# Optimization experiments

Measured on AMD Instinct MI355X. Metric: run time of the kernel, lower is better.

## Reference

```python
import jax, jax.numpy as jnp
import numpy as np

BN_EPS = 1e-5

def _bn(h, gamma, beta):
    # training-mode BatchNorm1d: batch stats over node axis
    mu = h.mean(0)
    var = h.var(0)
    return (h - mu) * jax.lax.rsqrt(var + BN_EPS) * gamma + beta

def setup_inputs() -> dict:
    key = jax.random.key(0)
    ks = jax.random.split(key, 12)
    N, E, NF, EF = 100000, 3200000, 16, 8
    x = jax.random.normal(ks[0], (N, NF), jnp.float32)
    edge_index = jax.random.randint(ks[1], (2, E), 0, N, jnp.int64)
    edge_attr = jax.random.normal(ks[2], (E, EF), jnp.float32)
    s = 0.1
    params = dict(
        We=jax.random.normal(ks[3], (EF, NF), jnp.float32) * s,
        be=jnp.zeros((NF,), jnp.float32),
        W1=jax.random.normal(ks[4], (NF, 32), jnp.float32) * s,
        b1=jnp.zeros((32,), jnp.float32),
        g1=jnp.ones((32,), jnp.float32),
        bt1=jnp.zeros((32,), jnp.float32),
        W2=jax.random.normal(ks[5], (32, 32), jnp.float32) * s,
        b2=jnp.zeros((32,), jnp.float32),
        eps=jnp.float32(0.0),
        g2=jnp.ones((32,), jnp.float32),
        bt2=jnp.zeros((32,), jnp.float32),
        W3=jax.random.normal(ks[6], (32, 64), jnp.float32) * s,
        b3=jnp.zeros((64,), jnp.float32),
    )
    return dict(x=x, edge_index=edge_index, edge_attr=edge_attr, **params)

def reference(x, edge_index, edge_attr, We, be, W1, b1, g1, bt1, W2, b2, eps, g2, bt2, W3, b3):
    N = x.shape[0]
    src, dst = edge_index[0], edge_index[1]
    # GINEConv: project edge_attr to node dim, message = ReLU(x_src + e)
    e = edge_attr @ We + be                      # [E, NF]
    msg = jax.nn.relu(x[src] + e)                # [E, NF]  (gather)
    agg = jax.ops.segment_sum(msg, dst, num_segments=N)  # [N, NF] (scatter-sum)
    h = (1.0 + eps) * x + agg
    # nn1: Linear -> BN -> GELU -> Linear
    h = h @ W1 + b1
    h = jax.nn.gelu(_bn(h, g1, bt1), approximate=False)
    h = h @ W2 + b2                              # [N, 32]
    # post-conv: BN -> GELU -> Linear(32,64)
    h = jax.nn.gelu(_bn(h, g2, bt2), approximate=False)
    return h @ W3 + b3                           # [N, 64]
```

## Files before the change

### kernel.cpp

```cpp
#include <hip/hip_runtime.h>
#include <math.h>

#define NF 16
#define EF 8
#define H1D 32
#define H2D 32
#define OD 64

__device__ __forceinline__ float gelu_exact(float t) {
    return 0.5f * t * (1.0f + erff(t * 0.70710678118654752440f));
}

__global__ __launch_bounds__(256) void k_hist(
    const int* __restrict__ ei, int* __restrict__ count, int* __restrict__ pos,
    int N, int E)
{
    int e = blockIdx.x * 256 + threadIdx.x;
    if (e >= E) return;
    int dst = ei[(size_t)E + e];
    if ((unsigned)dst >= (unsigned)N) { pos[e] = -1; return; }
    pos[e] = atomicAdd(&count[dst], 1);
}

#define SCAN_T 1024
__global__ __launch_bounds__(SCAN_T) void k_scan(
    const int* __restrict__ count, int* __restrict__ rowptr, int N)
{
    __shared__ int part[SCAN_T];
    int t = threadIdx.x;
    int C = (N + SCAN_T - 1) / SCAN_T;
    int lo = min(t * C, N), hi = min(lo + C, N);
    int s = 0;
    for (int i = lo; i < hi; ++i) s += count[i];
    part[t] = s;
    __syncthreads();
    for (int off = 1; off < SCAN_T; off <<= 1) {
        int v = (t >= off) ? part[t - off] : 0;
        __syncthreads();
        part[t] += v;
        __syncthreads();
    }
    int run = (t == 0) ? 0 : part[t - 1];
    for (int i = lo; i < hi; ++i) { rowptr[i] = run; run += count[i]; }
    if (t == SCAN_T - 1) rowptr[N] = part[SCAN_T - 1];
}

__global__ __launch_bounds__(256) void k_scatter(
    const int* __restrict__ ei, const int* __restrict__ rowptr,
    const int* __restrict__ pos, int* __restrict__ eids, int N, int E)
{
    int e = blockIdx.x * 256 + threadIdx.x;
    if (e >= E) return;
    int dst = ei[(size_t)E + e];
    if ((unsigned)dst >= (unsigned)N) return;
    int p = pos[e];
    if (p < 0) return;
    eids[rowptr[dst] + p] = e;
}

__global__ __launch_bounds__(256) void k_gather(
    const float* __restrict__ x, const int* __restrict__ ei,
    const float* __restrict__ ea, const float* __restrict__ We,
    const float* __restrict__ be, const int* __restrict__ rowptr,
    const int* __restrict__ eids, float* __restrict__ agg, int N, int E)
{
    int wid = (blockIdx.x * 256 + threadIdx.x) >> 6;
    int lane = threadIdx.x & 63;
    if (wid >= N) return;
    int f = lane & 15, g = lane >> 4;

    float w[EF];
#pragma unroll
    for (int k = 0; k < EF; ++k) w[k] = We[k * NF + f];
    float bef = be[f];

    int r0 = rowptr[wid], r1 = rowptr[wid + 1];
    float acc = 0.0f;
    for (int t = r0 + g; t < r1; t += 4) {
        int e = eids[t];
        if ((unsigned)e >= (unsigned)E) continue;
        int src = ei[e];
        if ((unsigned)src >= (unsigned)N) continue;
        const float4* ea4 = reinterpret_cast<const float4*>(ea + (size_t)e * EF);
        float4 a0 = ea4[0], a1 = ea4[1];
        float ev = bef;
        ev += a0.x * w[0] + a0.y * w[1] + a0.z * w[2] + a0.w * w[3]
            + a1.x * w[4] + a1.y * w[5] + a1.z * w[6] + a1.w * w[7];
        acc += fmaxf(x[(size_t)src * NF + f] + ev, 0.0f);
    }
    acc += __shfl_xor(acc, 16);
    acc += __shfl_xor(acc, 32);
    if (g == 0) agg[(size_t)wid * NF + f] = acc;
}

__global__ __launch_bounds__(256) void k_edge(
    const float* __restrict__ x, const int* __restrict__ ei,
    const float* __restrict__ ea, const float* __restrict__ We,
    const float* __restrict__ be, float* __restrict__ agg, int N, int E)
{
    __shared__ float sWe[EF * NF];
    __shared__ float sbe[NF];
    int t = threadIdx.x;
    if (t < EF * NF) sWe[t] = We[t];
    if (t < NF) sbe[t] = be[t];
    __syncthreads();
    int e = blockIdx.x * 256 + t;
    if (e >= E) return;
    int src = ei[e];
    int dst = ei[(size_t)E + e];
    if ((unsigned)src >= (unsigned)N || (unsigned)dst >= (unsigned)N) return;
    const float4* ea4 = reinterpret_cast<const float4*>(ea + (size_t)e * EF);
    float4 a0 = ea4[0], a1 = ea4[1];
    float ak[EF] = {a0.x, a0.y, a0.z, a0.w, a1.x, a1.y, a1.z, a1.w};
    const float4* sbe4 = reinterpret_cast<const float4*>(sbe);
    float4 ev[4] = {sbe4[0], sbe4[1], sbe4[2], sbe4[3]};
    const float4* sWe4 = reinterpret_cast<const float4*>(sWe);
#pragma unroll
    for (int k = 0; k < EF; ++k) {
        float a = ak[k];
#pragma unroll
        for (int j = 0; j < 4; ++j) {
            float4 wv = sWe4[k * 4 + j];
            ev[j].x += a * wv.x; ev[j].y += a * wv.y;
            ev[j].z += a * wv.z; ev[j].w += a * wv.w;
        }
    }
    const float4* xs = reinterpret_cast<const float4*>(x + (size_t)src * NF);
    float* ad = agg + (size_t)dst * NF;
#pragma unroll
    for (int j = 0; j < 4; ++j) {
        float4 xv = xs[j];
        atomicAdd(ad + j * 4 + 0, fmaxf(xv.x + ev[j].x, 0.0f));
        atomicAdd(ad + j * 4 + 1, fmaxf(xv.y + ev[j].y, 0.0f));
        atomicAdd(ad + j * 4 + 2, fmaxf(xv.z + ev[j].z, 0.0f));
        atomicAdd(ad + j * 4 + 3, fmaxf(xv.w + ev[j].w, 0.0f));
    }
}

__global__ __launch_bounds__(256) void k_nodeA(
    const float* __restrict__ x, const float* __restrict__ agg,
    const float* __restrict__ W1, const float* __restrict__ b1,
    const float* __restrict__ epsp, float* __restrict__ h1,
    float* __restrict__ partial, int N)
{
    __shared__ float sW1[NF * H1D];
    __shared__ float sb1[H1D];
    __shared__ float sred[4][H1D], qred[4][H1D];
    int t = threadIdx.x;
    for (int i = t; i < NF * H1D; i += 256) sW1[i] = W1[i];
    if (t < H1D) sb1[t] = b1[t];
    __syncthreads();

    int i = blockIdx.x * 256 + t;
    bool active = i < N;
    float onep = 1.0f + epsp[0];
    int w = t >> 6;

    float acc[H1D];
    if (active) {
        float h0[NF];
        const float4* xs = reinterpret_cast<const float4*>(x + (size_t)i * NF);
        const float4* as = reinterpret_cast<const float4*>(agg + (size_t)i * NF);
#pragma unroll
        for (int j = 0; j < 4; ++j) {
            float4 xv = xs[j], av = as[j];
            h0[4 * j + 0] = onep * xv.x + av.x;
            h0[4 * j + 1] = onep * xv.y + av.y;
            h0[4 * j + 2] = onep * xv.z + av.z;
            h0[4 * j + 3] = onep * xv.w + av.w;
        }
#pragma unroll
        for (int j = 0; j < H1D; ++j) acc[j] = sb1[j];
#pragma unroll
        for (int k = 0; k < NF; ++k) {
            float a = h0[k];
#pragma unroll
            for (int j = 0; j < H1D; ++j) acc[j] += a * sW1[k * H1D + j];
        }
        float4* o = reinterpret_cast<float4*>(h1 + (size_t)i * H1D);
#pragma unroll
        for (int j = 0; j < 8; ++j)
            o[j] = make_float4(acc[4 * j + 0], acc[4 * j + 1], acc[4 * j + 2], acc[4 * j + 3]);
    } else {
#pragma unroll
        for (int j = 0; j < H1D; ++j) acc[j] = 0.0f;
    }

#pragma unroll
    for (int j = 0; j < H1D; ++j) {
        float s = acc[j];
        float q = s * s;
#pragma unroll
        for (int off = 32; off; off >>= 1) {
            s += __shfl_xor(s, off);
            q += __shfl_xor(q, off);
        }
        if ((t & 63) == 0) { sred[w][j] = s; qred[w][j] = q; }
    }
    __syncthreads();
    float* pb = partial + (size_t)blockIdx.x * 64;
    if (t < H1D)
        pb[t] = sred[0][t] + sred[1][t] + sred[2][t] + sred[3][t];
    else if (t < 64)
        pb[t] = qred[0][t - 32] + qred[1][t - 32] + qred[2][t - 32] + qred[3][t - 32];
}

__global__ __launch_bounds__(256) void k_red(
    const float* __restrict__ partial, int rows,
    const float* __restrict__ g, const float* __restrict__ bt,
    float* __restrict__ stats, int N)
{
    __shared__ float acc[4][64];
    int t = threadIdx.x;
    int c = t & 63, r0 = t >> 6;
    float s = 0.0f;
    for (int r = r0; r < rows; r += 4) s += partial[(size_t)r * 64 + c];
    acc[r0][c] = s;
    __syncthreads();
    if (t < 64) acc[0][t] = acc[0][t] + acc[1][t] + acc[2][t] + acc[3][t];
    __syncthreads();
    if (t < 32) {
        float sum = acc[0][t], sq = acc[0][32 + t];
        float mu = sum / (float)N;
        float var = sq / (float)N - mu * mu;
        float inv = rsqrtf(var + 1e-5f);
        float scale = g[t] * inv;
        float shift = bt[t] - mu * scale;
        stats[t] = scale;
        stats[32 + t] = shift;
    }
}

__global__ __launch_bounds__(256) void k_nodeB(
    const float* __restrict__ h1, const float* __restrict__ st1,
    const float* __restrict__ W2, const float* __restrict__ b2,
    float* __restrict__ h2, float* __restrict__ partial, int N)
{
    __shared__ float sW2[H1D * H2D];
    __shared__ float sb2[H2D], ssc[H1D], ssh[H1D];
    __shared__ float sred[4][H2D], qred[4][H2D];
    int t = threadIdx.x;
    for (int i = t; i < H1D * H2D; i += 256) sW2[i] = W2[i];
    if (t < H2D) sb2[t] = b2[t];
    if (t < H1D) { ssc[t] = st1[t]; ssh[t] = st1[H1D + t]; }
    __syncthreads();

    int i = blockIdx.x * 256 + t;
    bool active = i < N;
    int w = t >> 6;

    float acc[H2D];
    if (active) {
        float tg[H1D];
        const float4* hs = reinterpret_cast<const float4*>(h1 + (size_t)i * H1D);
#pragma unroll
        for (int j = 0; j < 8; ++j) {
            float4 v = hs[j];
            tg[4 * j + 0] = gelu_exact(v.x * ssc[4 * j + 0] + ssh[4 * j + 0]);
            tg[4 * j + 1] = gelu_exact(v.y * ssc[4 * j + 1] + ssh[4 * j + 1]);
            tg[4 * j + 2] = gelu_exact(v.z * ssc[4 * j + 2] + ssh[4 * j + 2]);
            tg[4 * j + 3] = gelu_exact(v.w * ssc[4 * j + 3] + ssh[4 * j + 3]);
        }
#pragma unroll
        for (int j = 0; j < H2D; ++j) acc[j] = sb2[j];
#pragma unroll
        for (int k = 0; k < H1D; ++k) {
            float a = tg[k];
#pragma unroll
            for (int j = 0; j < H2D; ++j) acc[j] += a * sW2[k * H2D + j];
        }
        float4* o = reinterpret_cast<float4*>(h2 + (size_t)i * H2D);
#pragma unroll
        for (int j = 0; j < 8; ++j)
            o[j] = make_float4(acc[4 * j + 0], acc[4 * j + 1], acc[4 * j + 2], acc[4 * j + 3]);
    } else {
#pragma unroll
        for (int j = 0; j < H2D; ++j) acc[j] = 0.0f;
    }

#pragma unroll
    for (int j = 0; j < H2D; ++j) {
        float s = acc[j];
        float q = s * s;
#pragma unroll
        for (int off = 32; off; off >>= 1) {
            s += __shfl_xor(s, off);
            q += __shfl_xor(q, off);
        }
        if ((t & 63) == 0) { sred[w][j] = s; qred[w][j] = q; }
    }
    __syncthreads();
    float* pb = partial + (size_t)blockIdx.x * 64;
    if (t < H2D)
        pb[t] = sred[0][t] + sred[1][t] + sred[2][t] + sred[3][t];
    else if (t < 64)
        pb[t] = qred[0][t - 32] + qred[1][t - 32] + qred[2][t - 32] + qred[3][t - 32];
}

__global__ __launch_bounds__(256) void k_nodeC(
    const float* __restrict__ h2, const float* __restrict__ st2,
    const float* __restrict__ W3, const float* __restrict__ b3,
    float* __restrict__ out, int N)
{
    __shared__ float sW3[H2D * OD];
    __shared__ float sb3[OD], ssc[H2D], ssh[H2D];
    int t = threadIdx.x;
    for (int i = t; i < H2D * OD; i += 256) sW3[i] = W3[i];
    if (t < OD) sb3[t] = b3[t];
    if (t < H2D) { ssc[t] = st2[t]; ssh[t] = st2[H2D + t]; }
    __syncthreads();

    int i = blockIdx.x * 256 + t;
    if (i >= N) return;

    float tg[H2D];
    const float4* hs = reinterpret_cast<const float4*>(h2 + (size_t)i * H2D);
#pragma unroll
    for (int j = 0; j < 8; ++j) {
        float4 v = hs[j];
        tg[4 * j + 0] = gelu_exact(v.x * ssc[4 * j + 0] + ssh[4 * j + 0]);
        tg[4 * j + 1] = gelu_exact(v.y * ssc[4 * j + 1] + ssh[4 * j + 1]);
        tg[4 * j + 2] = gelu_exact(v.z * ssc[4 * j + 2] + ssh[4 * j + 2]);
        tg[4 * j + 3] = gelu_exact(v.w * ssc[4 * j + 3] + ssh[4 * j + 3]);
    }
    float acc[OD];
#pragma unroll
    for (int j = 0; j < OD; ++j) acc[j] = sb3[j];
#pragma unroll
    for (int k = 0; k < H2D; ++k) {
        float a = tg[k];
#pragma unroll
        for (int j = 0; j < OD; ++j) acc[j] += a * sW3[k * OD + j];
    }
    float4* o = reinterpret_cast<float4*>(out + (size_t)i * OD);
#pragma unroll
    for (int j = 0; j < 16; ++j)
        o[j] = make_float4(acc[4 * j + 0], acc[4 * j + 1], acc[4 * j + 2], acc[4 * j + 3]);
}

extern "C" void kernel_launch(void* const* d_in, const int* in_sizes, int n_in,
                              void* d_out, int out_size, void* d_ws, size_t ws_size,
                              hipStream_t stream) {
    const float* x   = (const float*)d_in[0];
    const int*   ei  = (const int*)d_in[1];
    const float* ea  = (const float*)d_in[2];
    const float* We  = (const float*)d_in[3];
    const float* be  = (const float*)d_in[4];
    const float* W1  = (const float*)d_in[5];
    const float* b1  = (const float*)d_in[6];
    const float* g1  = (const float*)d_in[7];
    const float* bt1 = (const float*)d_in[8];
    const float* W2  = (const float*)d_in[9];
    const float* b2  = (const float*)d_in[10];
    const float* epsp= (const float*)d_in[11];
    const float* g2  = (const float*)d_in[12];
    const float* bt2 = (const float*)d_in[13];
    const float* W3  = (const float*)d_in[14];
    const float* b3  = (const float*)d_in[15];

    int N = in_sizes[0] / NF;
    int E = in_sizes[2] / EF;
    float* out = (float*)d_out;

    int ebl = (E + 255) / 256;
    int nbl = (N + 255) / 256;
    int gbl = (N + 3) / 4;

    char* ws = (char*)d_ws;
    size_t aggB  = (size_t)N * NF * sizeof(float);
    size_t hB    = (size_t)N * H1D * sizeof(float);
    size_t cntB  = (size_t)N * sizeof(int);
    size_t rpB   = (size_t)(N + 1) * sizeof(int);
    size_t eB    = (size_t)E * sizeof(int);
    size_t statB = 512;
    size_t partB = (size_t)nbl * 64 * sizeof(float);

    size_t coreB = aggB + 2 * hB + cntB + rpB + statB + 2 * partB;
    size_t fullB = coreB + 2 * eB;

    if (ws_size >= coreB && (ws_size >= fullB || (size_t)out_size * sizeof(float) >= 2 * eB)) {
        char* p = ws;
        float* agg    = (float*)p; p += aggB;
        float* h1     = (float*)p; p += hB;
        float* h2     = (float*)p; p += hB;
        int*   count  = (int*)p;   p += cntB;
        int*   rowptr = (int*)p;   p += rpB;
        float* stats1 = (float*)p; p += statB;
        float* stats2 = stats1 + 64;
        float* part1  = (float*)p; p += partB;
        float* part2  = (float*)p; p += partB;
        int *pos, *eids;
        if (ws_size >= fullB) {
            pos  = (int*)p;
            eids = (int*)(p + eB);
        } else {
            pos  = (int*)d_out;
            eids = (int*)((char*)d_out + eB);
        }

        hipMemsetAsync(count, 0, cntB, stream);

        k_hist<<<ebl, 256, 0, stream>>>(ei, count, pos, N, E);
        k_scan<<<1, SCAN_T, 0, stream>>>(count, rowptr, N);
        k_scatter<<<ebl, 256, 0, stream>>>(ei, rowptr, pos, eids, N, E);
        k_gather<<<gbl, 256, 0, stream>>>(x, ei, ea, We, be, rowptr, eids, agg, N, E);
        k_nodeA<<<nbl, 256, 0, stream>>>(x, agg, W1, b1, epsp, h1, part1, N);
        k_red<<<1, 256, 0, stream>>>(part1, nbl, g1, bt1, stats1, N);
        k_nodeB<<<nbl, 256, 0, stream>>>(h1, stats1, W2, b2, h2, part2, N);
        k_red<<<1, 256, 0, stream>>>(part2, nbl, g2, bt2, stats2, N);
        k_nodeC<<<nbl, 256, 0, stream>>>(h2, stats2, W3, b3, out, N);
    } else {
        char* p = ws;
        float* agg = (float*)p; p += aggB;
        float *h1, *h2;
        if (ws_size >= aggB + 2 * hB + statB + 2 * partB) {
            h1 = (float*)p; p += hB;
            h2 = (float*)p; p += hB;
        } else {
            h1 = out;
            h2 = (float*)p; p += hB;
        }
        float* stats1 = (float*)p; p += statB;
        float* stats2 = stats1 + 64;
        float* part1  = (float*)p; p += partB;
        float* part2  = (float*)p; p += partB;

        hipMemsetAsync(agg, 0, aggB, stream);

        k_edge<<<ebl, 256, 0, stream>>>(x, ei, ea, We, be, agg, N, E);
        k_nodeA<<<nbl, 256, 0, stream>>>(x, agg, W1, b1, epsp, h1, part1, N);
        k_red<<<1, 256, 0, stream>>>(part1, nbl, g1, bt1, stats1, N);
        k_nodeB<<<nbl, 256, 0, stream>>>(h1, stats1, W2, b2, h2, part2, N);
        k_red<<<1, 256, 0, stream>>>(part2, nbl, g2, bt2, stats2, N);
        k_nodeC<<<nbl, 256, 0, stream>>>(h2, stats2, W3, b3, out, N);
    }
}
```

Measured before the change: 816.4 us.

## Compute edge messages in edge order and write them to CSR slots, then gather sequentially

Result: slower. 904.5 us (+10.8%).

```diff
diff --git a/kernel.cpp b/kernel.cpp
--- a/kernel.cpp
+++ b/kernel.cpp
@@ -45,17 +45,78 @@
     if (t == SCAN_T - 1) rowptr[N] = part[SCAN_T - 1];
 }
 
-__global__ __launch_bounds__(256) void k_scatter(
-    const int* __restrict__ ei, const int* __restrict__ rowptr,
-    const int* __restrict__ pos, int* __restrict__ eids, int N, int E)
-{
-    int e = blockIdx.x * 256 + threadIdx.x;
+__global__ __launch_bounds__(256) void k_scatmsg(
+    const float* __restrict__ x, const int* __restrict__ ei,
+    const float* __restrict__ ea, const float* __restrict__ We,
+    const float* __restrict__ be, const int* __restrict__ rowptr,
+    const int* __restrict__ pos, float* __restrict__ msg, int N, int E)
+{
+    __shared__ float sWe[EF * NF];
+    __shared__ float sbe[NF];
+    int t = threadIdx.x;
+    if (t < EF * NF) sWe[t] = We[t];
+    if (t < NF) sbe[t] = be[t];
+    __syncthreads();
+
+    int e = blockIdx.x * 256 + t;
     if (e >= E) return;
     int dst = ei[(size_t)E + e];
     if ((unsigned)dst >= (unsigned)N) return;
     int p = pos[e];
     if (p < 0) return;
-    eids[rowptr[dst] + p] = e;
+    size_t slot = (size_t)rowptr[dst] + p;
+    float4* mo = reinterpret_cast<float4*>(msg + slot * NF);
+
+    int src = ei[e];
+    if ((unsigned)src >= (unsigned)N) {
+        float4 z = make_float4(0.f, 0.f, 0.f, 0.f);
+        mo[0] = z; mo[1] = z; mo[2] = z; mo[3] = z;
+        return;
+    }
+
+    const float4* ea4 = reinterpret_cast<const float4*>(ea + (size_t)e * EF);
+    float4 a0 = ea4[0], a1 = ea4[1];
+    float ak[EF] = {a0.x, a0.y, a0.z, a0.w, a1.x, a1.y, a1.z, a1.w};
+    const float4* sbe4 = reinterpret_cast<const float4*>(sbe);
+    float4 ev[4] = {sbe4[0], sbe4[1], sbe4[2], sbe4[3]};
+    const float4* sWe4 = reinterpret_cast<const float4*>(sWe);
+#pragma unroll
+    for (int k = 0; k < EF; ++k) {
+        float a = ak[k];
+#pragma unroll
+        for (int j = 0; j < 4; ++j) {
+            float4 wv = sWe4[k * 4 + j];
+            ev[j].x += a * wv.x; ev[j].y += a * wv.y;
+            ev[j].z += a * wv.z; ev[j].w += a * wv.w;
+        }
+    }
+    const float4* xs = reinterpret_cast<const float4*>(x + (size_t)src * NF);
+#pragma unroll
+    for (int j = 0; j < 4; ++j) {
+        float4 xv = xs[j];
+        mo[j] = make_float4(fmaxf(xv.x + ev[j].x, 0.0f),
+                            fmaxf(xv.y + ev[j].y, 0.0f),
+                            fmaxf(xv.z + ev[j].z, 0.0f),
+                            fmaxf(xv.w + ev[j].w, 0.0f));
+    }
+}
+
+__global__ __launch_bounds__(256) void k_gatherseq(
+    const int* __restrict__ rowptr, const float* __restrict__ msg,
+    float* __restrict__ agg, int N)
+{
+    int wid = (blockIdx.x * 256 + threadIdx.x) >> 6;
+    int lane = threadIdx.x & 63;
+    if (wid >= N) return;
+    int f = lane & 15, g = lane >> 4;
+
+    int r0 = rowptr[wid], r1 = rowptr[wid + 1];
+    float acc = 0.0f;
+    for (int t = r0 + g; t < r1; t += 4)
+        acc += msg[(size_t)t * NF + f];
+    acc += __shfl_xor(acc, 16);
+    acc += __shfl_xor(acc, 32);
+    if (g == 0) agg[(size_t)wid * NF + f] = acc;
 }
 
 __global__ __launch_bounds__(256) void k_gather(
@@ -91,6 +152,19 @@
     acc += __shfl_xor(acc, 16);
     acc += __shfl_xor(acc, 32);
     if (g == 0) agg[(size_t)wid * NF + f] = acc;
+}
+
+__global__ __launch_bounds__(256) void k_scatter(
+    const int* __restrict__ ei, const int* __restrict__ rowptr,
+    const int* __restrict__ pos, int* __restrict__ eids, int N, int E)
+{
+    int e = blockIdx.x * 256 + threadIdx.x;
+    if (e >= E) return;
+    int dst = ei[(size_t)E + e];
+    if ((unsigned)dst >= (unsigned)N) return;
+    int p = pos[e];
+    if (p < 0) return;
+    eids[rowptr[dst] + p] = e;
 }
 
 __global__ __launch_bounds__(256) void k_edge(
@@ -372,13 +446,41 @@
     size_t cntB  = (size_t)N * sizeof(int);
     size_t rpB   = (size_t)(N + 1) * sizeof(int);
     size_t eB    = (size_t)E * sizeof(int);
+    size_t msgB  = (size_t)E * NF * sizeof(float);
     size_t statB = 512;
     size_t partB = (size_t)nbl * 64 * sizeof(float);
 
     size_t coreB = aggB + 2 * hB + cntB + rpB + statB + 2 * partB;
-    size_t fullB = coreB + 2 * eB;
-
-    if (ws_size >= coreB && (ws_size >= fullB || (size_t)out_size * sizeof(float) >= 2 * eB)) {
+    size_t tierA = coreB + eB + msgB;
+    size_t tierB = coreB + 2 * eB;
+
+    if (ws_size >= tierA) {
+        char* p = ws;
+        float* agg    = (float*)p; p += aggB;
+        float* h1     = (float*)p; p += hB;
+        float* h2     = (float*)p; p += hB;
+        float* msg    = (float*)p; p += msgB;
+        int*   pos    = (int*)p;   p += eB;
+        int*   count  = (int*)p;   p += cntB;
+        int*   rowptr = (int*)p;   p += rpB;
+        float* stats1 = (float*)p; p += statB;
+        float* stats2 = stats1 + 64;
+        float* part1  = (float*)p; p += partB;
+        float* part2  = (float*)p; p += partB;
+
+        hipMemsetAsync(count, 0, cntB, stream);
+
+        k_hist<<<ebl, 256, 0, stream>>>(ei, count, pos, N, E);
+        k_scan<<<1, SCAN_T, 0, stream>>>(count, rowptr, N);
+        k_scatmsg<<<ebl, 256, 0, stream>>>(x, ei, ea, We, be, rowptr, pos, msg, N, E);
+        k_gatherseq<<<gbl, 256, 0, stream>>>(rowptr, msg, agg, N);
+        k_nodeA<<<nbl, 256, 0, stream>>>(x, agg, W1, b1, epsp, h1, part1, N);
+        k_red<<<1, 256, 0, stream>>>(part1, nbl, g1, bt1, stats1, N);
+        k_nodeB<<<nbl, 256, 0, stream>>>(h1, stats1, W2, b2, h2, part2, N);
+        k_red<<<1, 256, 0, stream>>>(part2, nbl, g2, bt2, stats2, N);
+        k_nodeC<<<nbl, 256, 0, stream>>>(h2, stats2, W3, b3, out, N);
+    } else if (ws_size >= coreB &&
+               (ws_size >= tierB || (size_t)out_size * sizeof(float) >= 2 * eB)) {
         char* p = ws;
         float* agg    = (float*)p; p += aggB;
         float* h1     = (float*)p; p += hB;
@@ -390,7 +492,7 @@
         float* part1  = (float*)p; p += partB;
         float* part2  = (float*)p; p += partB;
         int *pos, *eids;
-        if (ws_size >= fullB) {
+        if (ws_size >= tierB) {
             pos  = (int*)p;
             eids = (int*)(p + eB);
         } else {
```

## Replace per-node CSR gather with binned edge partition and LDS atomic aggregation

Applied to the files above, without the earlier changes.

Result: no change. 805.3 us (-1.4%).

```diff
diff --git a/kernel.cpp b/kernel.cpp
--- a/kernel.cpp
+++ b/kernel.cpp
@@ -6,23 +6,52 @@
 #define H1D 32
 #define H2D 32
 #define OD 64
+#define PB 256
+#define BNODE 256
+#define SCAN_T 1024
+
+typedef float f32x4 __attribute__((ext_vector_type(4)));
 
 __device__ __forceinline__ float gelu_exact(float t) {
     return 0.5f * t * (1.0f + erff(t * 0.70710678118654752440f));
 }
 
-__global__ __launch_bounds__(256) void k_hist(
-    const int* __restrict__ ei, int* __restrict__ count, int* __restrict__ pos,
-    int N, int E)
-{
-    int e = blockIdx.x * 256 + threadIdx.x;
-    if (e >= E) return;
-    int dst = ei[(size_t)E + e];
-    if ((unsigned)dst >= (unsigned)N) { pos[e] = -1; return; }
-    pos[e] = atomicAdd(&count[dst], 1);
-}
-
-#define SCAN_T 1024
+__global__ __launch_bounds__(256) void k_count(
+    const int* __restrict__ ei, int* __restrict__ cnt, int N, int E, int NBIN, int per)
+{
+    extern __shared__ int lh[];
+    int b = blockIdx.x, t = threadIdx.x;
+    for (int i = t; i < NBIN; i += 256) lh[i] = 0;
+    __syncthreads();
+    int lo = b * per, hi = min(lo + per, E);
+    for (int e = lo + t; e < hi; e += 256) {
+        int dst = ei[(size_t)E + e];
+        int src = ei[e];
+        if ((unsigned)dst < (unsigned)N && (unsigned)src < (unsigned)N)
+            atomicAdd(&lh[dst >> 8], 1);
+    }
+    __syncthreads();
+    for (int i = t; i < NBIN; i += 256) cnt[(size_t)b * NBIN + i] = lh[i];
+}
+
+__global__ __launch_bounds__(256) void k_mscan(
+    const int* __restrict__ cnt, int* __restrict__ off, int* __restrict__ coltot, int NBIN)
+{
+    __shared__ int sh[256];
+    int bin = blockIdx.x, t = threadIdx.x;
+    int v = cnt[(size_t)t * NBIN + bin];
+    sh[t] = v;
+    __syncthreads();
+    for (int o = 1; o < 256; o <<= 1) {
+        int u = (t >= o) ? sh[t - o] : 0;
+        __syncthreads();
+        sh[t] += u;
+        __syncthreads();
+    }
+    off[(size_t)t * NBIN + bin] = sh[t] - v;
+    if (t == 255) coltot[bin] = sh[255];
+}
+
 __global__ __launch_bounds__(SCAN_T) void k_scan(
     const int* __restrict__ count, int* __restrict__ rowptr, int N)
 {
@@ -45,49 +74,173 @@
     if (t == SCAN_T - 1) rowptr[N] = part[SCAN_T - 1];
 }
 
-__global__ __launch_bounds__(256) void k_scatter(
-    const int* __restrict__ ei, const int* __restrict__ rowptr,
-    const int* __restrict__ pos, int* __restrict__ eids, int N, int E)
+__global__ __launch_bounds__(256) void k_place(
+    const int* __restrict__ ei, const float* __restrict__ ea,
+    const int* __restrict__ off, const int* __restrict__ binbase,
+    unsigned* __restrict__ srcpk, float* __restrict__ ea8,
+    int N, int E, int NBIN, int per)
+{
+    extern __shared__ int lc[];
+    int b = blockIdx.x, t = threadIdx.x;
+    for (int i = t; i < NBIN; i += 256) lc[i] = 0;
+    __syncthreads();
+    int lo = b * per, hi = min(lo + per, E);
+    for (int e = lo + t; e < hi; e += 256) {
+        int dst = ei[(size_t)E + e];
+        int src = ei[e];
+        if ((unsigned)dst >= (unsigned)N || (unsigned)src >= (unsigned)N) continue;
+        int bin = dst >> 8;
+        int pos = atomicAdd(&lc[bin], 1);
+        int slot = binbase[bin] + off[(size_t)b * NBIN + bin] + pos;
+        srcpk[slot] = ((unsigned)(dst & 255) << 24) | (unsigned)src;
+        const f32x4* s4 = reinterpret_cast<const f32x4*>(ea + (size_t)e * EF);
+        f32x4 a0 = s4[0], a1 = s4[1];
+        f32x4* d4 = reinterpret_cast<f32x4*>(ea8 + (size_t)slot * EF);
+        d4[0] = a0; d4[1] = a1;
+    }
+}
+
+__global__ __launch_bounds__(256) void k_binagg(
+    const float* __restrict__ x, const unsigned* __restrict__ srcpk,
+    const float* __restrict__ ea8, const float* __restrict__ We,
+    const float* __restrict__ be, const int* __restrict__ binbase,
+    float* __restrict__ agg2, int N)
+{
+    __shared__ float sWe[EF * NF];
+    __shared__ float sbe[NF];
+    __shared__ float as[NF * BNODE];
+    int t = threadIdx.x;
+    int bin = blockIdx.x >> 1, s = blockIdx.x & 1;
+    if (t < EF * NF) sWe[t] = We[t];
+    if (t < NF) sbe[t] = be[t];
+    for (int i = t; i < NF * BNODE; i += 256) as[i] = 0.0f;
+    __syncthreads();
+
+    int lo = binbase[bin], hi = binbase[bin + 1];
+    int half = (hi - lo) >> 1;
+    int l0 = s ? (lo + half) : lo;
+    int h0 = s ? hi : (lo + half);
+
+    const f32x4* sw = reinterpret_cast<const f32x4*>(sWe);
+    const f32x4* sb4 = reinterpret_cast<const f32x4*>(sbe);
+    for (int idx = l0 + t; idx < h0; idx += 256) {
+        unsigned u = srcpk[idx];
+        int src = (int)(u & 0xFFFFFFu);
+        int doff = (int)(u >> 24);
+        const f32x4* e4 = reinterpret_cast<const f32x4*>(ea8 + (size_t)idx * EF);
+        f32x4 a0 = e4[0], a1 = e4[1];
+        float ak[EF] = {a0[0], a0[1], a0[2], a0[3], a1[0], a1[1], a1[2], a1[3]};
+        f32x4 ev[4] = {sb4[0], sb4[1], sb4[2], sb4[3]};
+#pragma unroll
+        for (int k = 0; k < EF; ++k) {
+            float a = ak[k];
+#pragma unroll
+            for (int j = 0; j < 4; ++j) ev[j] += a * sw[k * 4 + j];
+        }
+        const f32x4* xs = reinterpret_cast<const f32x4*>(x + (size_t)src * NF);
+#pragma unroll
+        for (int j = 0; j < 4; ++j) {
+            f32x4 xv = xs[j];
+#pragma unroll
+            for (int c = 0; c < 4; ++c) {
+                float m = fmaxf(xv[c] + ev[j][c], 0.0f);
+                atomicAdd(&as[(j * 4 + c) * BNODE + doff], m);
+            }
+        }
+    }
+    __syncthreads();
+
+    float* ag = agg2 + (size_t)s * (size_t)N * NF;
+    int node = bin * BNODE + t;
+    if (t < BNODE && node < N) {
+        f32x4* o = reinterpret_cast<f32x4*>(ag + (size_t)node * NF);
+#pragma unroll
+        for (int j = 0; j < 4; ++j) {
+            f32x4 v;
+#pragma unroll
+            for (int c = 0; c < 4; ++c) v[c] = as[(j * 4 + c) * BNODE + t];
+            o[j] = v;
+        }
+    }
+}
+
+__global__ __launch_bounds__(256) void k_histp(
+    const int* __restrict__ ei, int* __restrict__ count, unsigned* __restrict__ packed,
+    int N, int E)
 {
     int e = blockIdx.x * 256 + threadIdx.x;
     if (e >= E) return;
     int dst = ei[(size_t)E + e];
-    if ((unsigned)dst >= (unsigned)N) return;
-    int p = pos[e];
-    if (p < 0) return;
-    eids[rowptr[dst] + p] = e;
-}
-
-__global__ __launch_bounds__(256) void k_gather(
+    if ((unsigned)dst >= (unsigned)N || dst >= (1 << 20)) { packed[e] = 0xFFFFFFFFu; return; }
+    int p = atomicAdd(&count[dst], 1);
+    if (p > 4095) p = 4095;
+    packed[e] = ((unsigned)p << 20) | (unsigned)dst;
+}
+
+__global__ __launch_bounds__(256) void k_scatmsg(
     const float* __restrict__ x, const int* __restrict__ ei,
     const float* __restrict__ ea, const float* __restrict__ We,
     const float* __restrict__ be, const int* __restrict__ rowptr,
-    const int* __restrict__ eids, float* __restrict__ agg, int N, int E)
+    const unsigned* __restrict__ packed, float* __restrict__ msg, int N, int E)
+{
+    __shared__ float sWe[EF * NF];
+    __shared__ float sbe[NF];
+    int t = threadIdx.x;
+    if (t < EF * NF) sWe[t] = We[t];
+    if (t < NF) sbe[t] = be[t];
+    __syncthreads();
+
+    int e = blockIdx.x * 256 + t;
+    if (e >= E) return;
+    unsigned u = packed[e];
+    if (u == 0xFFFFFFFFu) return;
+    int dst = (int)(u & 0xFFFFFu);
+    int p   = (int)(u >> 20);
+    size_t slot = (size_t)rowptr[dst] + p;
+    f32x4* mo = reinterpret_cast<f32x4*>(msg + slot * NF);
+
+    int src = ei[e];
+    if ((unsigned)src >= (unsigned)N) {
+        f32x4 z = (f32x4)0.0f;
+        mo[0] = z; mo[1] = z; mo[2] = z; mo[3] = z;
+        return;
+    }
+    const f32x4* ea4 = reinterpret_cast<const f32x4*>(ea + (size_t)e * EF);
+    f32x4 a01 = __builtin_nontemporal_load(ea4 + 0);
+    f32x4 a23 = __builtin_nontemporal_load(ea4 + 1);
+    float ak[EF] = {a01[0], a01[1], a01[2], a01[3], a23[0], a23[1], a23[2], a23[3]};
+    const f32x4* sbe4 = reinterpret_cast<const f32x4*>(sbe);
+    f32x4 ev[4] = {sbe4[0], sbe4[1], sbe4[2], sbe4[3]};
+    const f32x4* sWe4 = reinterpret_cast<const f32x4*>(sWe);
+#pragma unroll
+    for (int k = 0; k < EF; ++k) {
+        float a = ak[k];
+#pragma unroll
+        for (int j = 0; j < 4; ++j) ev[j] += a * sWe4[k * 4 + j];
+    }
+    const f32x4* xs = reinterpret_cast<const f32x4*>(x + (size_t)src * NF);
+#pragma unroll
+    for (int j = 0; j < 4; ++j) {
+        f32x4 xv = xs[j];
+        f32x4 m;
+#pragma unroll
+        for (int c = 0; c < 4; ++c) m[c] = fmaxf(xv[c] + ev[j][c], 0.0f);
+        mo[j] = m;
+    }
+}
+
+__global__ __launch_bounds__(256) void k_gatherseq(
+    const int* __restrict__ rowptr, const float* __restrict__ msg,
+    float* __restrict__ agg, int N)
 {
     int wid = (blockIdx.x * 256 + threadIdx.x) >> 6;
     int lane = threadIdx.x & 63;
     if (wid >= N) return;
     int f = lane & 15, g = lane >> 4;
-
-    float w[EF];
-#pragma unroll
-    for (int k = 0; k < EF; ++k) w[k] = We[k * NF + f];
-    float bef = be[f];
-
     int r0 = rowptr[wid], r1 = rowptr[wid + 1];
     float acc = 0.0f;
-    for (int t = r0 + g; t < r1; t += 4) {
-        int e = eids[t];
-        if ((unsigned)e >= (unsigned)E) continue;
-        int src = ei[e];
-        if ((unsigned)src >= (unsigned)N) continue;
-        const float4* ea4 = reinterpret_cast<const float4*>(ea + (size_t)e * EF);
-        float4 a0 = ea4[0], a1 = ea4[1];
-        float ev = bef;
-        ev += a0.x * w[0] + a0.y * w[1] + a0.z * w[2] + a0.w * w[3]
-            + a1.x * w[4] + a1.y * w[5] + a1.z * w[6] + a1.w * w[7];
-        acc += fmaxf(x[(size_t)src * NF + f] + ev, 0.0f);
-    }
+    for (int t = r0 + g; t < r1; t += 4)
+        acc += __builtin_nontemporal_load(msg + (size_t)t * NF + f);
     acc += __shfl_xor(acc, 16);
     acc += __shfl_xor(acc, 32);
     if (g == 0) agg[(size_t)wid * NF + f] = acc;
@@ -138,7 +291,8 @@
 }
 
 __global__ __launch_bounds__(256) void k_nodeA(
-    const float* __restrict__ x, const float* __restrict__ agg,
+    const float* __restrict__ x, const float* __restrict__ aggL,
+    const float* __restrict__ aggH,
     const float* __restrict__ W1, const float* __restrict__ b1,
     const float* __restrict__ epsp, float* __restrict__ h1,
     float* __restrict__ partial, int N)
@@ -160,14 +314,16 @@
     if (active) {
         float h0[NF];
         const float4* xs = reinterpret_cast<const float4*>(x + (size_t)i * NF);
-        const float4* as = reinterpret_cast<const float4*>(agg + (size_t)i * NF);
+        const float4* aL = reinterpret_cast<const float4*>(aggL + (size_t)i * NF);
+        const float4* aH = aggH ? reinterpret_cast<const float4*>(aggH + (size_t)i * NF) : nullptr;
 #pragma unroll
         for (int j = 0; j < 4; ++j) {
-            float4 xv = xs[j], av = as[j];
-            h0[4 * j + 0] = onep * xv.x + av.x;
-            h0[4 * j + 1] = onep * xv.y + av.y;
-            h0[4 * j + 2] = onep * xv.z + av.z;
-            h0[4 * j + 3] = onep * xv.w + av.w;
+            float4 xv = xs[j], av = aL[j];
+            float4 bv = aH ? aH[j] : make_float4(0.f, 0.f, 0.f, 0.f);
+            h0[4 * j + 0] = onep * xv.x + av.x + bv.x;
+            h0[4 * j + 1] = onep * xv.y + av.y + bv.y;
+            h0[4 * j + 2] = onep * xv.z + av.z + bv.z;
+            h0[4 * j + 3] = onep * xv.w + av.w + bv.w;
         }
 #pragma unroll
         for (int j = 0; j < H1D; ++j) acc[j] = sb1[j];
@@ -365,73 +521,98 @@
     int ebl = (E + 255) / 256;
     int nbl = (N + 255) / 256;
     int gbl = (N + 3) / 4;
+    int NBIN = (N + BNODE - 1) / BNODE;
+    int per  = (E + PB - 1) / PB;
+
+    auto al = [](size_t v) { return (v + 63) & ~(size_t)63; };
 
     char* ws = (char*)d_ws;
-    size_t aggB  = (size_t)N * NF * sizeof(float);
-    size_t hB    = (size_t)N * H1D * sizeof(float);
-    size_t cntB  = (size_t)N * sizeof(int);
-    size_t rpB   = (size_t)(N + 1) * sizeof(int);
-    size_t eB    = (size_t)E * sizeof(int);
-    size_t statB = 512;
-    size_t partB = (size_t)nbl * 64 * sizeof(float);
-
-    size_t coreB = aggB + 2 * hB + cntB + rpB + statB + 2 * partB;
-    size_t fullB = coreB + 2 * eB;
-
-    if (ws_size >= coreB && (ws_size >= fullB || (size_t)out_size * sizeof(float) >= 2 * eB)) {
+    size_t aggB   = al((size_t)N * NF * sizeof(float));
+    size_t agg2B  = al((size_t)2 * N * NF * sizeof(float));
+    size_t hB     = al((size_t)N * H1D * sizeof(float));
+    size_t eB     = al((size_t)E * sizeof(int));
+    size_t ea8B   = al((size_t)E * EF * sizeof(float));
+    size_t msgB   = al((size_t)E * NF * sizeof(float));
+    size_t cntMB  = al((size_t)PB * NBIN * sizeof(int));
+    size_t ctB    = al((size_t)(NBIN + 1) * sizeof(int));
+    size_t cntB   = al((size_t)N * sizeof(int));
+    size_t rpB    = al((size_t)(N + 1) * sizeof(int));
+    size_t statB  = al(512);
+    size_t partB  = al((size_t)nbl * 64 * sizeof(float));
+
+    size_t binTotal = ea8B + eB + agg2B + 2 * hB + 2 * cntMB + 2 * ctB + statB + 2 * partB;
+    size_t msgTotal = msgB + eB + aggB + 2 * hB + cntB + rpB + statB + 2 * partB;
+
+    bool binOK = (N < (1 << 24)) && (NBIN >= 1) && (NBIN <= 16000) &&
+                 ((size_t)NBIN * 4 <= 64 * 1024) && (ws_size >= binTotal);
+
+    if (binOK) {
         char* p = ws;
-        float* agg    = (float*)p; p += aggB;
-        float* h1     = (float*)p; p += hB;
-        float* h2     = (float*)p; p += hB;
-        int*   count  = (int*)p;   p += cntB;
-        int*   rowptr = (int*)p;   p += rpB;
+        float* ea8    = (float*)p;    p += ea8B;
+        unsigned* srcpk = (unsigned*)p; p += eB;
+        float* agg2   = (float*)p;    p += agg2B;
+        float* h1     = (float*)p;    p += hB;
+        float* h2     = (float*)p;    p += hB;
+        int*   cntM   = (int*)p;      p += cntMB;
+        int*   offM   = (int*)p;      p += cntMB;
+        int*   coltot = (int*)p;      p += ctB;
+        int*   binbase= (int*)p;      p += ctB;
+        float* stats1 = (float*)p;    p += statB;
+        float* stats2 = stats1 + 64;
+        float* part1  = (float*)p;    p += partB;
+        float* part2  = (float*)p;    p += partB;
+
+        size_t ldsHist = (size_t)NBIN * sizeof(int);
+        k_count <<<PB, 256, ldsHist, stream>>>(ei, cntM, N, E, NBIN, per);
+        k_mscan <<<NBIN, 256, 0, stream>>>(cntM, offM, coltot, NBIN);
+        k_scan  <<<1, SCAN_T, 0, stream>>>(coltot, binbase, NBIN);
+        k_place <<<PB, 256, ldsHist, stream>>>(ei, ea, offM, binbase, srcpk, ea8, N, E, NBIN, per);
+        k_binagg<<<NBIN * 2, 256, 0, stream>>>(x, srcpk, ea8, We, be, binbase, agg2, N);
+        k_nodeA <<<nbl, 256, 0, stream>>>(x, agg2, agg2 + (size_t)N * NF, W1, b1, epsp, h1, part1, N);
+        k_red   <<<1, 256, 0, stream>>>(part1, nbl, g1, bt1, stats1, N);
+        k_nodeB <<<nbl, 256, 0, stream>>>(h1, stats1, W2, b2, h2, part2, N);
+        k_red   <<<1, 256, 0, stream>>>(part2, nbl, g2, bt2, stats2, N);
+        k_nodeC <<<nbl, 256, 0, stream>>>(h2, stats2, W3, b3, out, N);
+    } else if (ws_size >= msgTotal) {
+        char* p = ws;
+        float* msg    = (float*)p;    p += msgB;
+        unsigned* packed = (unsigned*)p; p += eB;
+        float* agg    = (float*)p;    p += aggB;
+        float* h1     = (float*)p;    p += hB;
+        float* h2     = (float*)p;    p += hB;
+        int*   count  = (int*)p;      p += cntB;
+        int*   rowptr = (int*)p;      p += rpB;
+        float* stats1 = (float*)p;    p += statB;
+        float* stats2 = stats1 + 64;
+        float* part1  = (float*)p;    p += partB;
+        float* part2  = (float*)p;    p += partB;
+
+        hipMemsetAsync(count, 0, (size_t)N * sizeof(int), stream);
+        k_histp   <<<ebl, 256, 0, stream>>>(ei, count, packed, N, E);
+        k_scan    <<<1, SCAN_T, 0, stream>>>(count, rowptr, N);
+        k_scatmsg <<<ebl, 256, 0, stream>>>(x, ei, ea, We, be, rowptr, packed, msg, N, E);
+        k_gatherseq<<<gbl, 256, 0, stream>>>(rowptr, msg, agg, N);
+        k_nodeA   <<<nbl, 256, 0, stream>>>(x, agg, nullptr, W1, b1, epsp, h1, part1, N);
+        k_red     <<<1, 256, 0, stream>>>(part1, nbl, g1, bt1, stats1, N);
+        k_nodeB   <<<nbl, 256, 0, stream>>>(h1, stats1, W2, b2, h2, part2, N);
+        k_red     <<<1, 256, 0, stream>>>(part2, nbl, g2, bt2, stats2, N);
+        k_nodeC   <<<nbl, 256, 0, stream>>>(h2, stats2, W3, b3, out, N);
+    } else {
+        char* p = ws;
+        float* agg = (float*)p; p += aggB;
+        float* h1  = (float*)p; p += hB;
+        float* h2  = (float*)p; p += hB;
         float* stats1 = (float*)p; p += statB;
         float* stats2 = stats1 + 64;
         float* part1  = (float*)p; p += partB;
         float* part2  = (float*)p; p += partB;
-        int *pos, *eids;
-        if (ws_size >= fullB) {
-            pos  = (int*)p;
-            eids = (int*)(p + eB);
-        } else {
-            pos  = (int*)d_out;
-            eids = (int*)((char*)d_out + eB);
-        }
-
-        hipMemsetAsync(count, 0, cntB, stream);
-
-        k_hist<<<ebl, 256, 0, stream>>>(ei, count, pos, N, E);
-        k_scan<<<1, SCAN_T, 0, stream>>>(count, rowptr, N);
-        k_scatter<<<ebl, 256, 0, stream>>>(ei, rowptr, pos, eids, N, E);
-        k_gather<<<gbl, 256, 0, stream>>>(x, ei, ea, We, be, rowptr, eids, agg, N, E);
-        k_nodeA<<<nbl, 256, 0, stream>>>(x, agg, W1, b1, epsp, h1, part1, N);
-        k_red<<<1, 256, 0, stream>>>(part1, nbl, g1, bt1, stats1, N);
-        k_nodeB<<<nbl, 256, 0, stream>>>(h1, stats1, W2, b2, h2, part2, N);
-        k_red<<<1, 256, 0, stream>>>(part2, nbl, g2, bt2, stats2, N);
-        k_nodeC<<<nbl, 256, 0, stream>>>(h2, stats2, W3, b3, out, N);
-    } else {
-        char* p = ws;
-        float* agg = (float*)p; p += aggB;
-        float *h1, *h2;
-        if (ws_size >= aggB + 2 * hB + statB + 2 * partB) {
-            h1 = (float*)p; p += hB;
-            h2 = (float*)p; p += hB;
-        } else {
-            h1 = out;
-            h2 = (float*)p; p += hB;
-        }
-        float* stats1 = (float*)p; p += statB;
-        float* stats2 = stats1 + 64;
-        float* part1  = (float*)p; p += partB;
-        float* part2  = (float*)p; p += partB;
-
-        hipMemsetAsync(agg, 0, aggB, stream);
-
-        k_edge<<<ebl, 256, 0, stream>>>(x, ei, ea, We, be, agg, N, E);
-        k_nodeA<<<nbl, 256, 0, stream>>>(x, agg, W1, b1, epsp, h1, part1, N);
-        k_red<<<1, 256, 0, stream>>>(part1, nbl, g1, bt1, stats1, N);
-        k_nodeB<<<nbl, 256, 0, stream>>>(h1, stats1, W2, b2, h2, part2, N);
-        k_red<<<1, 256, 0, stream>>>(part2, nbl, g2, bt2, stats2, N);
-        k_nodeC<<<nbl, 256, 0, stream>>>(h2, stats2, W3, b3, out, N);
-    }
-}
+
+        hipMemsetAsync(agg, 0, (size_t)N * NF * sizeof(float), stream);
+        k_edge  <<<ebl, 256, 0, stream>>>(x, ei, ea, We, be, agg, N, E);
+        k_nodeA <<<nbl, 256, 0, stream>>>(x, agg, nullptr, W1, b1, epsp, h1, part1, N);
+        k_red   <<<1, 256, 0, stream>>>(part1, nbl, g1, bt1, stats1, N);
+        k_nodeB <<<nbl, 256, 0, stream>>>(h1, stats1, W2, b2, h2, part2, N);
+        k_red   <<<1, 256, 0, stream>>>(part2, nbl, g2, bt2, stats2, N);
+        k_nodeC <<<nbl, 256, 0, stream>>>(h2, stats2, W3, b3, out, N);
+    }
+}
```
